# Optimization experiments

Hardware: AMD Instinct MI355X
Metric: run time of the kernel (lower is better)

## Reference

```python
import jax, jax.numpy as jnp
import numpy as np

D_MODEL = 1024
NUM_HEADS = 16
WINDOW = 256
HEAD_DIM = D_MODEL // NUM_HEADS


def setup_inputs() -> dict:
    key = jax.random.key(0)
    ks = jax.random.split(key, 5)
    B, L, D = 2, 2048, D_MODEL
    s = 1.0 / np.sqrt(D)
    x = jax.random.normal(ks[0], (B, L, D), dtype=jnp.float32)
    w_qkv = jax.random.normal(ks[1], (3 * D, D), dtype=jnp.float32) * s
    b_qkv = jnp.zeros((3 * D,), dtype=jnp.float32)
    w_proj = jax.random.normal(ks[2], (D, D), dtype=jnp.float32) * s
    b_proj = jnp.zeros((D,), dtype=jnp.float32)
    return {"x": x, "w_qkv": w_qkv, "b_qkv": b_qkv, "w_proj": w_proj, "b_proj": b_proj}


def reference(x, w_qkv, b_qkv, w_proj, b_proj):
    B, L, D = x.shape
    H, E = NUM_HEADS, HEAD_DIM
    scale = 1.0 / jnp.sqrt(jnp.asarray(E, dtype=x.dtype))
    # torch Linear: y = x @ W.T + b
    qkv = (x @ w_qkv.T + b_qkv).reshape(B, L, 3, H, E)
    qkv = jnp.transpose(qkv, (2, 0, 3, 1, 4))  # [3, B, H, L, E]
    q, k, v = qkv[0], qkv[1], qkv[2]
    scores = jnp.einsum('bhle,bhme->bhlm', q, k) * scale  # [B,H,L,L]
    i = jnp.arange(L)[:, None]
    j = jnp.arange(L)[None, :]
    mask = (j > i) | ((i - j) >= WINDOW)  # causal OR outside window
    scores = jnp.where(mask, jnp.asarray(-10000.0, dtype=scores.dtype), scores)
    attn = jax.nn.softmax(scores, axis=-1)
    out = jnp.einsum('bhlm,bhme->bhle', attn, v)  # [B,H,L,E]
    out = jnp.transpose(out, (0, 2, 1, 3)).reshape(B, L, D)
    return out @ w_proj.T + b_proj
```

## Files before the change

kernel.cpp:

```cpp
#include <hip/hip_runtime.h>

typedef __bf16 bf16x8 __attribute__((ext_vector_type(8)));
typedef float f32x4 __attribute__((ext_vector_type(4)));
typedef unsigned short u16;
typedef unsigned int u32;

__device__ __forceinline__ u16 f2bf(float f) {
  u32 u = __builtin_bit_cast(u32, f);
  u32 r = (u + 0x7FFFu + ((u >> 16) & 1u)) >> 16;
  return (u16)r;
}

__device__ __forceinline__ void gload16(const u16* g, u16* lds_base) {
  __builtin_amdgcn_global_load_lds(
      (const __attribute__((address_space(1))) void*)g,
      (__attribute__((address_space(3))) void*)lds_base, 16, 0, 0);
}

__global__ void cast_all(const float* __restrict__ x,  u16* __restrict__ xo,
                         const float* __restrict__ wq, u16* __restrict__ wqo,
                         const float* __restrict__ wp, u16* __restrict__ wpo) {
  const int NX = (2 * 2048 * 1024) / 4;
  const int NQ = (3072 * 1024) / 4;
  const int NP = (1024 * 1024) / 4;
  int i = blockIdx.x * blockDim.x + threadIdx.x;
  int stride = gridDim.x * blockDim.x;
  for (; i < NX + NQ + NP; i += stride) {
    const float4* s; uint2* d; int j;
    if (i < NX)            { s = (const float4*)x;  d = (uint2*)xo;  j = i; }
    else if (i < NX + NQ)  { s = (const float4*)wq; d = (uint2*)wqo; j = i - NX; }
    else                   { s = (const float4*)wp; d = (uint2*)wpo; j = i - NX - NQ; }
    float4 f = s[j];
    uint2 o;
    o.x = (u32)f2bf(f.x) | ((u32)f2bf(f.y) << 16);
    o.y = (u32)f2bf(f.z) | ((u32)f2bf(f.w) << 16);
    d[j] = o;
  }
}

template<int OUT_BF16, int BM, int BN>
__global__ __launch_bounds__(256) void gemm_nt(
    const u16* __restrict__ A, const u16* __restrict__ W,
    const float* __restrict__ bias, void* __restrict__ Cout,
    int M, int N, int K)
{
  constexpr int MT = BM / 32;
  constexpr int NT = BN / 32;
  __shared__ u16 Alds[2][BM][32];
  __shared__ u16 Blds[2][BN][32];
  const int tid  = threadIdx.x;
  const int lane = tid & 63;
  const int wave = tid >> 6;
  const int wm = (wave >> 1) * (BM / 2);
  const int wn = (wave & 1) * (BN / 2);

  const int b    = blockIdx.x;
  const int xcd  = b & 7;
  const int slot = b >> 3;
  const int npx  = (N / BN) >> 3;
  const int m0 = (slot / npx) * BM;
  const int n0 = (xcd * npx + slot % npx) * BN;

  const int quad = lane >> 4;
  const int li   = lane & 15;

  const u16* ga = &A[(size_t)(m0 + wave * (BM / 4) + (lane >> 2)) * K + (lane & 3) * 8];
  const u16* gb = &W[(size_t)(n0 + wave * (BN / 4) + (lane >> 2)) * K + (lane & 3) * 8];

  auto stage = [&](int buf, int k0) {
#pragma unroll
    for (int i = 0; i < BM / 64; i++)
      gload16(ga + (size_t)i * 16 * K + k0, &Alds[buf][wave * (BM / 4) + i * 16][0]);
#pragma unroll
    for (int i = 0; i < BN / 64; i++)
      gload16(gb + (size_t)i * 16 * K + k0, &Blds[buf][wave * (BN / 4) + i * 16][0]);
  };

  f32x4 acc[MT][NT] = {};
  const int niter = K / 32;

  stage(0, 0);

#pragma unroll 2
  for (int kt = 0; kt < niter; kt++) {
    __syncthreads();
    if (kt + 1 < niter) stage((kt + 1) & 1, (kt + 1) * 32);
    const int buf = kt & 1;
    bf16x8 af[MT], bfr[NT];
#pragma unroll
    for (int t = 0; t < MT; t++)
      af[t] = *(const bf16x8*)&Alds[buf][wm + t * 16 + li][quad * 8];
#pragma unroll
    for (int t = 0; t < NT; t++)
      bfr[t] = *(const bf16x8*)&Blds[buf][wn + t * 16 + li][quad * 8];
#pragma unroll
    for (int mt = 0; mt < MT; mt++)
#pragma unroll
      for (int nt = 0; nt < NT; nt++)
        acc[mt][nt] = __builtin_amdgcn_mfma_f32_16x16x32_bf16(af[mt], bfr[nt], acc[mt][nt], 0, 0, 0);
  }

#pragma unroll
  for (int mt = 0; mt < MT; mt++)
#pragma unroll
    for (int nt = 0; nt < NT; nt++) {
      int gn = n0 + wn + nt * 16 + li;
      float bv = bias[gn];
#pragma unroll
      for (int r = 0; r < 4; r++) {
        int gm = m0 + wm + mt * 16 + quad * 4 + r;
        float v = acc[mt][nt][r] + bv;
        if (OUT_BF16)
          ((u16*)Cout)[(size_t)gm * N + gn] = f2bf(v);
        else
          ((float*)Cout)[(size_t)gm * N + gn] = v;
      }
    }
}

__global__ __launch_bounds__(256, 4) void attn_kernel(const u16* __restrict__ qkv,
                                                      u16* __restrict__ aout)
{
  const int L = 2048, DQ = 3072, D = 1024;
  const int q0 = blockIdx.x * 64;
  const int h  = blockIdx.y;
  const int b  = blockIdx.z;
  const int tid  = threadIdx.x;
  const int lane = tid & 63;
  const int wave = tid >> 6;
  const int quad = lane >> 4;
  const int li   = lane & 15;

  __shared__ u16 Klds[64][68];
  __shared__ u16 Vt[64][68];
  __shared__ u16 Plds[4][16][68];

  const u16* base = qkv + (size_t)b * L * DQ + h * 64;

  bf16x8 qf[2];
  {
    const u16* qsrc = base + (size_t)(q0 + wave * 16 + li) * DQ;
    qf[0] = *(const bf16x8*)&qsrc[quad * 8];
    qf[1] = *(const bf16x8*)&qsrc[32 + quad * 8];
  }

  f32x4 O[4] = {};
  float lsum[4] = {0.f, 0.f, 0.f, 0.f};

  const float scale = 0.125f;
  const int gq = q0 + wave * 16 + quad * 4;

  const int sr2 = (tid >> 3) * 2, sc = (tid & 7) * 8;
  const u16* ksbase = base + D;
  const u16* vsbase = base + 2 * D;
  uint4 kr0, kr1, vr0, vr1;
  auto loadkv = [&](int t) {
    int kb = q0 - 256 + t * 64;
    const u16* ks = ksbase + (size_t)kb * DQ;
    const u16* vs = vsbase + (size_t)kb * DQ;
    kr0 = *(const uint4*)&ks[(size_t)sr2 * DQ + sc];
    kr1 = *(const uint4*)&ks[(size_t)(sr2 + 1) * DQ + sc];
    vr0 = *(const uint4*)&vs[(size_t)sr2 * DQ + sc];
    vr1 = *(const uint4*)&vs[(size_t)(sr2 + 1) * DQ + sc];
  };

  const int t0 = (blockIdx.x < 4) ? (4 - (int)blockIdx.x) : 0;
  loadkv(t0);

  for (int t = t0; t < 5; t++) {
    const int kb = q0 - 256 + t * 64;
    __syncthreads();
    *(uint4*)&Klds[sr2][sc]     = kr0;
    *(uint4*)&Klds[sr2 + 1][sc] = kr1;
    {
      u32 a0[4] = {vr0.x, vr0.y, vr0.z, vr0.w};
      u32 a1[4] = {vr1.x, vr1.y, vr1.z, vr1.w};
#pragma unroll
      for (int j2 = 0; j2 < 4; j2++) {
        u32 lo0 = a0[j2] & 0xffffu, hi0 = a0[j2] >> 16;
        u32 lo1 = a1[j2] & 0xffffu, hi1 = a1[j2] >> 16;
        *(u32*)&Vt[sc + 2 * j2][sr2]     = lo0 | (lo1 << 16);
        *(u32*)&Vt[sc + 2 * j2 + 1][sr2] = hi0 | (hi1 << 16);
      }
    }
    __syncthreads();
    if (t + 1 < 5) loadkv(t + 1);

    f32x4 sacc[4] = {};
#pragma unroll
    for (int nt = 0; nt < 4; nt++) {
      bf16x8 kf0 = *(const bf16x8*)&Klds[nt * 16 + li][quad * 8];
      bf16x8 kf1 = *(const bf16x8*)&Klds[nt * 16 + li][32 + quad * 8];
      sacc[nt] = __builtin_amdgcn_mfma_f32_16x16x32_bf16(qf[0], kf0, sacc[nt], 0, 0, 0);
      sacc[nt] = __builtin_amdgcn_mfma_f32_16x16x32_bf16(qf[1], kf1, sacc[nt], 0, 0, 0);
    }

#pragma unroll
    for (int nt = 0; nt < 4; nt++) {
      int gj = kb + nt * 16 + li;
#pragma unroll
      for (int r = 0; r < 4; r++) {
        bool masked = (gj > gq + r) || ((gq + r) - gj >= 256);
        float p = masked ? 0.f : __expf(sacc[nt][r] * scale - 12.f);
        lsum[r] += p;
        Plds[wave][quad * 4 + r][nt * 16 + li] = f2bf(p);
      }
    }

    bf16x8 pf0 = *(const bf16x8*)&Plds[wave][li][quad * 8];
    bf16x8 pf1 = *(const bf16x8*)&Plds[wave][li][32 + quad * 8];
#pragma unroll
    for (int nt = 0; nt < 4; nt++) {
      bf16x8 vb0 = *(const bf16x8*)&Vt[nt * 16 + li][quad * 8];
      bf16x8 vb1 = *(const bf16x8*)&Vt[nt * 16 + li][32 + quad * 8];
      O[nt] = __builtin_amdgcn_mfma_f32_16x16x32_bf16(pf0, vb0, O[nt], 0, 0, 0);
      O[nt] = __builtin_amdgcn_mfma_f32_16x16x32_bf16(pf1, vb1, O[nt], 0, 0, 0);
    }
  }

#pragma unroll
  for (int d = 1; d < 16; d <<= 1)
#pragma unroll
    for (int r = 0; r < 4; r++)
      lsum[r] += __shfl_xor(lsum[r], d, 64);
#pragma unroll
  for (int r = 0; r < 4; r++) {
    float inv = 1.f / lsum[r];
#pragma unroll
    for (int nt = 0; nt < 4; nt++)
      aout[(size_t)(b * L + gq + r) * D + h * 64 + nt * 16 + li] = f2bf(O[nt][r] * inv);
  }
}

extern "C" void kernel_launch(void* const* d_in, const int* in_sizes, int n_in,
                              void* d_out, int out_size, void* d_ws, size_t ws_size,
                              hipStream_t stream) {
  const float* x      = (const float*)d_in[0];
  const float* w_qkv  = (const float*)d_in[1];
  const float* b_qkv  = (const float*)d_in[2];
  const float* w_proj = (const float*)d_in[3];
  const float* b_proj = (const float*)d_in[4];
  float* out = (float*)d_out;

  char* ws = (char*)d_ws;
  u16* x_bf     = (u16*)(ws);
  u16* wqkv_bf  = (u16*)(ws + ((size_t)8  << 20));
  u16* wproj_bf = (u16*)(ws + ((size_t)14 << 20));
  u16* qkv_bf   = (u16*)(ws + ((size_t)16 << 20));
  u16* attn_bf  = (u16*)(ws + ((size_t)40 << 20));

  cast_all<<<1024, 256, 0, stream>>>(x, x_bf, w_qkv, wqkv_bf, w_proj, wproj_bf);

  gemm_nt<1, 128, 128><<<(4096 / 128) * (3072 / 128), 256, 0, stream>>>(
      x_bf, wqkv_bf, b_qkv, qkv_bf, 4096, 3072, 1024);

  attn_kernel<<<dim3(2048 / 64, 16, 2), 256, 0, stream>>>(qkv_bf, attn_bf);

  gemm_nt<0, 128, 128><<<(4096 / 128) * (1024 / 128), 256, 0, stream>>>(
      attn_bf, wproj_bf, b_proj, out, 4096, 1024, 1024);
}
```

Baseline: 162.6 us.

## Add 256x256 swizzled-LDS GEMM for QKV projection; retile output projection

Adds a new 512-thread GEMM kernel for the QKV projection. It uses 256x256 output tiles, a 64-wide K step, an XOR-swizzled LDS layout to avoid bank conflicts, double-buffered direct global-to-LDS loads with explicit barriers, and raised priority around the MFMA bursts. The goal is more data reuse per tile and better overlap of loads with MFMA work. It also switches the output projection GEMM to 128x64 tiles so more blocks run for the smaller N. The trade-off is a grid of only 192 blocks for the QKV GEMM, which may not fill all CUs, plus high register and LDS use.

```diff
diff --git a/kernel.cpp b/kernel.cpp
--- a/kernel.cpp
+++ b/kernel.cpp
@@ -38,6 +38,102 @@
   }
 }
 
+__global__ __launch_bounds__(512, 2) void gemm256(
+    const u16* __restrict__ A, const u16* __restrict__ W,
+    const float* __restrict__ bias, u16* __restrict__ Cout,
+    int M, int N, int K)
+{
+  __shared__ u16 Alds[2][256][64];
+  __shared__ u16 Blds[2][256][64];
+  const int tid  = threadIdx.x;
+  const int lane = tid & 63;
+  const int wave = tid >> 6;
+  const int wm128 = (wave >> 2) * 128;
+  const int wn64  = (wave & 3) * 64;
+  const int quad = lane >> 4;
+  const int li   = lane & 15;
+  const int swz  = (li & 7) * 8;
+
+  const int b = blockIdx.x;
+  const int wgid = (b & 7) * 24 + (b >> 3);
+  const int m0 = (wgid & 15) * 256;
+  const int n0 = (wgid >> 4) * 256;
+
+  const int srow = lane >> 3;
+  const int sblk = (lane & 7) ^ srow;
+  const u16* gaBase = A + (size_t)(m0 + wave * 32 + srow) * K + sblk * 8;
+  const u16* gbBase = W + (size_t)(n0 + wave * 32 + srow) * K + sblk * 8;
+
+  auto stage = [&](int buf, int k0) {
+#pragma unroll
+    for (int c = 0; c < 4; ++c)
+      gload16(gaBase + (size_t)(c * 8) * K + k0, &Alds[buf][wave * 32 + c * 8][0]);
+#pragma unroll
+    for (int c = 0; c < 4; ++c)
+      gload16(gbBase + (size_t)(c * 8) * K + k0, &Blds[buf][wave * 32 + c * 8][0]);
+  };
+
+  f32x4 acc[8][4] = {};
+  const int NT16 = K >> 6;
+
+  stage(0, 0);
+  asm volatile("s_waitcnt vmcnt(0)" ::: "memory");
+  __builtin_amdgcn_s_barrier();
+
+  for (int t = 0; t < NT16; ++t) {
+    const int buf = t & 1;
+    bf16x8 bfr[4][2];
+#pragma unroll
+    for (int sp = 0; sp < 4; ++sp) {
+      bf16x8 af[2][2];
+#pragma unroll
+      for (int mi = 0; mi < 2; ++mi)
+#pragma unroll
+        for (int k = 0; k < 2; ++k)
+          af[mi][k] = *(const bf16x8*)
+              &Alds[buf][wm128 + (2 * sp + mi) * 16 + li][(quad * 8 + k * 32) ^ swz];
+      if (sp == 0) {
+#pragma unroll
+        for (int nf = 0; nf < 4; ++nf)
+#pragma unroll
+          for (int k = 0; k < 2; ++k)
+            bfr[nf][k] = *(const bf16x8*)
+                &Blds[buf][wn64 + nf * 16 + li][(quad * 8 + k * 32) ^ swz];
+        if (t + 1 < NT16) stage(buf ^ 1, (t + 1) * 64);
+      }
+      __builtin_amdgcn_s_barrier();
+      asm volatile("s_waitcnt lgkmcnt(0)" ::: "memory");
+      __builtin_amdgcn_sched_barrier(0);
+      __builtin_amdgcn_s_setprio(1);
+#pragma unroll
+      for (int mi = 0; mi < 2; ++mi)
+#pragma unroll
+        for (int nf = 0; nf < 4; ++nf)
+#pragma unroll
+          for (int k = 0; k < 2; ++k)
+            acc[2 * sp + mi][nf] = __builtin_amdgcn_mfma_f32_16x16x32_bf16(
+                af[mi][k], bfr[nf][k], acc[2 * sp + mi][nf], 0, 0, 0);
+      __builtin_amdgcn_s_setprio(0);
+      if (sp == 3) asm volatile("s_waitcnt vmcnt(0)" ::: "memory");
+      __builtin_amdgcn_s_barrier();
+    }
+  }
+
+#pragma unroll
+  for (int nf = 0; nf < 4; ++nf) {
+    int gn = n0 + wn64 + nf * 16 + li;
+    float bv = bias[gn];
+#pragma unroll
+    for (int mf = 0; mf < 8; ++mf) {
+#pragma unroll
+      for (int r = 0; r < 4; ++r) {
+        int gm = m0 + wm128 + mf * 16 + quad * 4 + r;
+        Cout[(size_t)gm * N + gn] = f2bf(acc[mf][nf][r] + bv);
+      }
+    }
+  }
+}
+
 template<int OUT_BF16, int BM, int BN>
 __global__ __launch_bounds__(256) void gemm_nt(
     const u16* __restrict__ A, const u16* __restrict__ W,
@@ -251,11 +347,11 @@
 
   cast_all<<<1024, 256, 0, stream>>>(x, x_bf, w_qkv, wqkv_bf, w_proj, wproj_bf);
 
-  gemm_nt<1, 128, 128><<<(4096 / 128) * (3072 / 128), 256, 0, stream>>>(
+  gemm256<<<(4096 / 256) * (3072 / 256), 512, 0, stream>>>(
       x_bf, wqkv_bf, b_qkv, qkv_bf, 4096, 3072, 1024);
 
   attn_kernel<<<dim3(2048 / 64, 16, 2), 256, 0, stream>>>(qkv_bf, attn_bf);
 
-  gemm_nt<0, 128, 128><<<(4096 / 128) * (1024 / 128), 256, 0, stream>>>(
+  gemm_nt<0, 128, 64><<<(4096 / 128) * (1024 / 64), 256, 0, stream>>>(
       attn_bf, wproj_bf, b_proj, out, 4096, 1024, 1024);
 }
```

Result: slower. 167.2 us (+2.8%).

## Load K fragments directly from global and double-buffer V tile to drop a barrier

Applied to the files above, without the earlier changes.

The attention kernel no longer stages K through shared memory. Each wave reads its K MFMA fragments straight from global memory (L2/cache), so the K LDS buffer and its stores go away. V transposed tiles are double-buffered in LDS, which lets the loop drop the leading __syncthreads so there is one barrier per iteration instead of two. In exchange, each of the four waves re-reads the same K tile from global memory, and the K loads are no longer prefetched one iteration ahead, so their latency sits directly in front of the QK MFMAs.

```diff
diff --git a/kernel.cpp b/kernel.cpp
--- a/kernel.cpp
+++ b/kernel.cpp
@@ -131,8 +131,7 @@
   const int quad = lane >> 4;
   const int li   = lane & 15;
 
-  __shared__ u16 Klds[64][68];
-  __shared__ u16 Vt[64][68];
+  __shared__ u16 Vt[2][64][68];
   __shared__ u16 Plds[4][16][68];
 
   const u16* base = qkv + (size_t)b * L * DQ + h * 64;
@@ -153,25 +152,20 @@
   const int sr2 = (tid >> 3) * 2, sc = (tid & 7) * 8;
   const u16* ksbase = base + D;
   const u16* vsbase = base + 2 * D;
-  uint4 kr0, kr1, vr0, vr1;
-  auto loadkv = [&](int t) {
+  uint4 vr0, vr1;
+  auto loadv = [&](int t) {
     int kb = q0 - 256 + t * 64;
-    const u16* ks = ksbase + (size_t)kb * DQ;
     const u16* vs = vsbase + (size_t)kb * DQ;
-    kr0 = *(const uint4*)&ks[(size_t)sr2 * DQ + sc];
-    kr1 = *(const uint4*)&ks[(size_t)(sr2 + 1) * DQ + sc];
     vr0 = *(const uint4*)&vs[(size_t)sr2 * DQ + sc];
     vr1 = *(const uint4*)&vs[(size_t)(sr2 + 1) * DQ + sc];
   };
 
   const int t0 = (blockIdx.x < 4) ? (4 - (int)blockIdx.x) : 0;
-  loadkv(t0);
+  loadv(t0);
 
   for (int t = t0; t < 5; t++) {
     const int kb = q0 - 256 + t * 64;
-    __syncthreads();
-    *(uint4*)&Klds[sr2][sc]     = kr0;
-    *(uint4*)&Klds[sr2 + 1][sc] = kr1;
+    const int vb = t & 1;
     {
       u32 a0[4] = {vr0.x, vr0.y, vr0.z, vr0.w};
       u32 a1[4] = {vr1.x, vr1.y, vr1.z, vr1.w};
@@ -179,18 +173,20 @@
       for (int j2 = 0; j2 < 4; j2++) {
         u32 lo0 = a0[j2] & 0xffffu, hi0 = a0[j2] >> 16;
         u32 lo1 = a1[j2] & 0xffffu, hi1 = a1[j2] >> 16;
-        *(u32*)&Vt[sc + 2 * j2][sr2]     = lo0 | (lo1 << 16);
-        *(u32*)&Vt[sc + 2 * j2 + 1][sr2] = hi0 | (hi1 << 16);
+        *(u32*)&Vt[vb][sc + 2 * j2][sr2]     = lo0 | (lo1 << 16);
+        *(u32*)&Vt[vb][sc + 2 * j2 + 1][sr2] = hi0 | (hi1 << 16);
       }
     }
     __syncthreads();
-    if (t + 1 < 5) loadkv(t + 1);
-
+    if (t + 1 < 5) loadv(t + 1);
+
+    const u16* ks = ksbase + (size_t)kb * DQ;
     f32x4 sacc[4] = {};
 #pragma unroll
     for (int nt = 0; nt < 4; nt++) {
-      bf16x8 kf0 = *(const bf16x8*)&Klds[nt * 16 + li][quad * 8];
-      bf16x8 kf1 = *(const bf16x8*)&Klds[nt * 16 + li][32 + quad * 8];
+      const u16* kr = ks + (size_t)(nt * 16 + li) * DQ;
+      bf16x8 kf0 = *(const bf16x8*)&kr[quad * 8];
+      bf16x8 kf1 = *(const bf16x8*)&kr[32 + quad * 8];
       sacc[nt] = __builtin_amdgcn_mfma_f32_16x16x32_bf16(qf[0], kf0, sacc[nt], 0, 0, 0);
       sacc[nt] = __builtin_amdgcn_mfma_f32_16x16x32_bf16(qf[1], kf1, sacc[nt], 0, 0, 0);
     }
@@ -211,8 +207,8 @@
     bf16x8 pf1 = *(const bf16x8*)&Plds[wave][li][32 + quad * 8];
 #pragma unroll
     for (int nt = 0; nt < 4; nt++) {
-      bf16x8 vb0 = *(const bf16x8*)&Vt[nt * 16 + li][quad * 8];
-      bf16x8 vb1 = *(const bf16x8*)&Vt[nt * 16 + li][32 + quad * 8];
+      bf16x8 vb0 = *(const bf16x8*)&Vt[vb][nt * 16 + li][quad * 8];
+      bf16x8 vb1 = *(const bf16x8*)&Vt[vb][nt * 16 + li][32 + quad * 8];
       O[nt] = __builtin_amdgcn_mfma_f32_16x16x32_bf16(pf0, vb0, O[nt], 0, 0, 0);
       O[nt] = __builtin_amdgcn_mfma_f32_16x16x32_bf16(pf1, vb1, O[nt], 0, 0, 0);
     }
```

New measurement: 170.4 us. 1.05x slower.

## Double attention query tile to 128 rows with 8 waves and XCD-aware block mapping

Applied to the files above, without the earlier changes.

The attention kernel now processes 128 query rows per workgroup using 512 threads (8 waves), so each K/V tile loaded into LDS is reused by twice as many queries. The grid becomes a flat 512 blocks remapped so consecutive blocks on an XCD share batch/head, improving L2 locality. Each 128-row block iterates 6 key tiles instead of 5, and there are half as many blocks, which lowers occupancy and adds some fully masked work per block in exchange for less redundant K/V loading.

```diff
diff --git a/kernel.cpp b/kernel.cpp
--- a/kernel.cpp
+++ b/kernel.cpp
@@ -118,13 +118,16 @@
     }
 }
 
-__global__ __launch_bounds__(256, 4) void attn_kernel(const u16* __restrict__ qkv,
+__global__ __launch_bounds__(512, 4) void attn_kernel(const u16* __restrict__ qkv,
                                                       u16* __restrict__ aout)
 {
   const int L = 2048, DQ = 3072, D = 1024;
-  const int q0 = blockIdx.x * 64;
-  const int h  = blockIdx.y;
-  const int b  = blockIdx.z;
+  const int bid  = blockIdx.x;
+  const int wgid = (bid & 7) * 64 + (bid >> 3);
+  const int qt = wgid & 15;
+  const int h  = (wgid >> 4) & 15;
+  const int b  = wgid >> 8;
+  const int q0 = qt * 128;
   const int tid  = threadIdx.x;
   const int lane = tid & 63;
   const int wave = tid >> 6;
@@ -133,7 +136,7 @@
 
   __shared__ u16 Klds[64][68];
   __shared__ u16 Vt[64][68];
-  __shared__ u16 Plds[4][16][68];
+  __shared__ u16 Plds[8][16][68];
 
   const u16* base = qkv + (size_t)b * L * DQ + h * 64;
 
@@ -150,41 +153,38 @@
   const float scale = 0.125f;
   const int gq = q0 + wave * 16 + quad * 4;
 
-  const int sr2 = (tid >> 3) * 2, sc = (tid & 7) * 8;
+  const int sr = tid >> 3, sc = (tid & 7) * 8;
+  const int srv = (tid >> 4) * 2, scv = (tid & 15) * 4;
   const u16* ksbase = base + D;
   const u16* vsbase = base + 2 * D;
-  uint4 kr0, kr1, vr0, vr1;
+  uint4 kr; uint2 vr0, vr1;
   auto loadkv = [&](int t) {
     int kb = q0 - 256 + t * 64;
-    const u16* ks = ksbase + (size_t)kb * DQ;
-    const u16* vs = vsbase + (size_t)kb * DQ;
-    kr0 = *(const uint4*)&ks[(size_t)sr2 * DQ + sc];
-    kr1 = *(const uint4*)&ks[(size_t)(sr2 + 1) * DQ + sc];
-    vr0 = *(const uint4*)&vs[(size_t)sr2 * DQ + sc];
-    vr1 = *(const uint4*)&vs[(size_t)(sr2 + 1) * DQ + sc];
+    kr  = *(const uint4*)&ksbase[(size_t)(kb + sr) * DQ + sc];
+    vr0 = *(const uint2*)&vsbase[(size_t)(kb + srv) * DQ + scv];
+    vr1 = *(const uint2*)&vsbase[(size_t)(kb + srv + 1) * DQ + scv];
   };
 
-  const int t0 = (blockIdx.x < 4) ? (4 - (int)blockIdx.x) : 0;
+  const int t0 = (qt == 0) ? 4 : (qt == 1) ? 2 : 0;
   loadkv(t0);
 
-  for (int t = t0; t < 5; t++) {
+  for (int t = t0; t < 6; t++) {
     const int kb = q0 - 256 + t * 64;
     __syncthreads();
-    *(uint4*)&Klds[sr2][sc]     = kr0;
-    *(uint4*)&Klds[sr2 + 1][sc] = kr1;
+    *(uint4*)&Klds[sr][sc] = kr;
     {
-      u32 a0[4] = {vr0.x, vr0.y, vr0.z, vr0.w};
-      u32 a1[4] = {vr1.x, vr1.y, vr1.z, vr1.w};
-#pragma unroll
-      for (int j2 = 0; j2 < 4; j2++) {
+      u32 a0[2] = {vr0.x, vr0.y};
+      u32 a1[2] = {vr1.x, vr1.y};
+#pragma unroll
+      for (int j2 = 0; j2 < 2; j2++) {
         u32 lo0 = a0[j2] & 0xffffu, hi0 = a0[j2] >> 16;
         u32 lo1 = a1[j2] & 0xffffu, hi1 = a1[j2] >> 16;
-        *(u32*)&Vt[sc + 2 * j2][sr2]     = lo0 | (lo1 << 16);
-        *(u32*)&Vt[sc + 2 * j2 + 1][sr2] = hi0 | (hi1 << 16);
+        *(u32*)&Vt[scv + 2 * j2][srv]     = lo0 | (lo1 << 16);
+        *(u32*)&Vt[scv + 2 * j2 + 1][srv] = hi0 | (hi1 << 16);
       }
     }
     __syncthreads();
-    if (t + 1 < 5) loadkv(t + 1);
+    if (t + 1 < 6) loadkv(t + 1);
 
     f32x4 sacc[4] = {};
 #pragma unroll
@@ -254,7 +254,7 @@
   gemm_nt<1, 128, 128><<<(4096 / 128) * (3072 / 128), 256, 0, stream>>>(
       x_bf, wqkv_bf, b_qkv, qkv_bf, 4096, 3072, 1024);
 
-  attn_kernel<<<dim3(2048 / 64, 16, 2), 256, 0, stream>>>(qkv_bf, attn_bf);
+  attn_kernel<<<512, 512, 0, stream>>>(qkv_bf, attn_bf);
 
   gemm_nt<0, 128, 128><<<(4096 / 128) * (1024 / 128), 256, 0, stream>>>(
       attn_bf, wproj_bf, b_proj, out, 4096, 1024, 1024);
```

Result: no change. 159.7 us (-1.8%).
